# Kernel optimization log

Measured on AMD Instinct MI355X. Metric: run time of the kernel, lower is better.

The kernel has to match this reference:

```python
import jax, jax.numpy as jnp
import numpy as np

EPS = 1e-08


def setup_inputs() -> dict:
    key = jax.random.key(0)
    k1, = jax.random.split(key, 1)
    B, T, F = 64, 1000, 257
    mag = jax.random.uniform(k1, (B, T, F), dtype=jnp.float32)
    s = jnp.zeros((B, F), dtype=jnp.float32)
    weights = jnp.ones((1, 1, F), dtype=jnp.float32)
    bias = jnp.zeros((1, 1, F), dtype=jnp.float32)
    alpha = jnp.full((1, F), -4.0, dtype=jnp.float32)
    return {"mag": mag, "s": s, "weights": weights, "bias": bias, "alpha": alpha}


def reference(mag, s, weights, bias, alpha):
    # mag: [B, T, F]; s: [B, F] initial EMA state
    power = mag * mag                      # [B, T, F]
    a = jax.nn.sigmoid(alpha)              # [1, F], broadcasts over B

    def step(carry, p_t):
        # carry: [B, F], p_t: [B, F]
        new = carry * (1.0 - a) + p_t * a
        return new, new

    # scan over time axis: move T to leading axis
    _, smooth = jax.lax.scan(step, s, jnp.swapaxes(power, 0, 1))  # smooth: [T, B, F]
    smooth_data = jnp.sqrt(jnp.swapaxes(smooth, 0, 1))            # [B, T, F]
    return mag / (smooth_data + EPS) * weights + bias
```

## Files before the change

kernel.cpp:

```cpp
#include <hip/hip_runtime.h>

#define EPS 1e-8f

__device__ __forceinline__ float sigmoidf_(float x) {
    return 1.0f / (1.0f + expf(-x));
}


template <int L>
__global__ __launch_bounds__(256)
void fns12_aggregate(const float* __restrict__ mag,
                     const float* __restrict__ alpha,
                     float* __restrict__ S,
                     int B, int T, int F, int C1) {
    const int BF = B * F;
    int g = blockIdx.x * blockDim.x + threadIdx.x;
    if (g >= BF * C1) return;
    const int bf = g % BF;
    const int c  = g / BF;
    const int b  = bf / F;
    const int f  = bf - b * F;

    const float a   = sigmoidf_(alpha[f]);
    const float oma = 1.0f - a;

    const float* p = mag + ((size_t)b * T + (size_t)c * L) * F + f;

    float m[L];
#pragma unroll
    for (int t = 0; t < L; ++t)
        m[t] = p[(size_t)t * F];
    asm volatile("" ::: "memory");

    float local = 0.0f;
#pragma unroll
    for (int t = 0; t < L; ++t)
        local = local * oma + (m[t] * m[t]) * a;
    S[(size_t)c * BF + bf] = local;
}

template <int L, int C>
__global__ __launch_bounds__(256)
void fns12_emit(const float* __restrict__ mag,
                const float* __restrict__ s0,
                const float* __restrict__ weights,
                const float* __restrict__ bias,
                const float* __restrict__ alpha,
                const float* __restrict__ S,
                float* __restrict__ out,
                int B, int T, int F) {
    const int BF = B * F;
    int g = blockIdx.x * blockDim.x + threadIdx.x;
    if (g >= BF * C) return;
    const int bf = g % BF;
    const int c  = g / BF;
    const int b  = bf / F;
    const int f  = bf - b * F;

    const float a   = sigmoidf_(alpha[f]);
    const float oma = 1.0f - a;
    const float w   = weights[f];
    const float bi  = bias[f];

    const float* p = mag + ((size_t)b * T + (size_t)c * L) * F + f;
    float*       o = out + ((size_t)b * T + (size_t)c * L) * F + f;

    float m[L];
#pragma unroll
    for (int t = 0; t < L; ++t)
        m[t] = p[(size_t)t * F];

    float SS[C - 1];
#pragma unroll
    for (int j = 0; j < C - 1; ++j)
        SS[j] = (j < c) ? S[(size_t)j * BF + bf] : 0.0f;
    asm volatile("" ::: "memory");

    float D = 1.0f;
#pragma unroll
    for (int i = 0; i < L; ++i) D *= oma;
    float carry = s0[bf];
#pragma unroll
    for (int j = 0; j < C - 1; ++j)
        carry = (j < c) ? (carry * D + SS[j]) : carry;

#pragma unroll
    for (int t = 0; t < L; ++t) {
        carry = carry * oma + (m[t] * m[t]) * a;
        o[(size_t)t * F] = m[t] * __builtin_amdgcn_rcpf(sqrtf(carry) + EPS) * w + bi;
    }
}

template <int L>
__global__ __launch_bounds__(256)
void fns11_emit(const float* __restrict__ mag,
                const float* __restrict__ s0,
                const float* __restrict__ weights,
                const float* __restrict__ bias,
                const float* __restrict__ alpha,
                const float* __restrict__ S,
                float* __restrict__ out,
                int B, int T, int F, int C) {
    const int BF = B * F;
    int g = blockIdx.x * blockDim.x + threadIdx.x;
    if (g >= BF * C) return;
    const int bf = g % BF;
    const int c  = g / BF;
    const int b  = bf / F;
    const int f  = bf - b * F;

    const float a   = sigmoidf_(alpha[f]);
    const float oma = 1.0f - a;
    const float w   = weights[f];
    const float bi  = bias[f];

    float carry = s0[bf];
    if (c > 0) {
        float D = 1.0f;
#pragma unroll
        for (int i = 0; i < L; ++i) D *= oma;
        for (int j = 0; j < c; ++j)
            carry = carry * D + S[(size_t)j * BF + bf];
    }

    const float* p = mag + ((size_t)b * T + (size_t)c * L) * F + f;
    float*       o = out + ((size_t)b * T + (size_t)c * L) * F + f;

    float m[L];
#pragma unroll
    for (int t = 0; t < L; ++t)
        m[t] = p[(size_t)t * F];
    asm volatile("" ::: "memory");

#pragma unroll
    for (int t = 0; t < L; ++t) {
        carry = carry * oma + (m[t] * m[t]) * a;
        o[(size_t)t * F] = m[t] * __builtin_amdgcn_rcpf(sqrtf(carry) + EPS) * w + bi;
    }
}

__global__ void fns_fallback(const float* __restrict__ mag,
                             const float* __restrict__ s0,
                             const float* __restrict__ weights,
                             const float* __restrict__ bias,
                             const float* __restrict__ alpha,
                             float* __restrict__ out,
                             int B, int T, int F) {
    int bf = blockIdx.x * blockDim.x + threadIdx.x;
    int BF = B * F;
    if (bf >= BF) return;
    int b = bf / F;
    int f = bf - b * F;

    float a  = sigmoidf_(alpha[f]);
    float w  = weights[f];
    float bi = bias[f];

    float carry = s0[bf];
    const float* p = mag + (size_t)b * T * F + f;
    float*       o = out + (size_t)b * T * F + f;

    for (int t = 0; t < T; ++t) {
        float m = p[(size_t)t * F];
        carry = carry * (1.0f - a) + (m * m) * a;
        o[(size_t)t * F] = m / (sqrtf(carry) + EPS) * w + bi;
    }
}

extern "C" void kernel_launch(void* const* d_in, const int* in_sizes, int n_in,
                              void* d_out, int out_size, void* d_ws, size_t ws_size,
                              hipStream_t stream) {
    const float* mag     = (const float*)d_in[0];
    const float* s0      = (const float*)d_in[1];
    const float* weights = (const float*)d_in[2];
    const float* bias    = (const float*)d_in[3];
    const float* alpha   = (const float*)d_in[4];
    float* out = (float*)d_out;

    int F  = in_sizes[4];
    int BF = in_sizes[1];
    int B  = BF / F;
    int T  = in_sizes[0] / BF;

    constexpr int L = 50;
    if (T % L == 0) {
        int C  = T / L;
        int C1 = C - 1;
        size_t need = (size_t)C1 * BF * sizeof(float);
        if (C1 >= 1 && ws_size >= need) {
            float* S = (float*)d_ws;
            int n1 = BF * C1;
            int n2 = BF * C;
            fns12_aggregate<L><<<(n1 + 255) / 256, 256, 0, stream>>>(
                mag, alpha, S, B, T, F, C1);
            if (C == 20) {
                fns12_emit<L, 20><<<(n2 + 255) / 256, 256, 0, stream>>>(
                    mag, s0, weights, bias, alpha, S, out, B, T, F);
            } else {
                fns11_emit<L><<<(n2 + 255) / 256, 256, 0, stream>>>(
                    mag, s0, weights, bias, alpha, S, out, B, T, F, C);
            }
            return;
        }
    }

    int threads = 256;
    int blocks  = (BF + threads - 1) / threads;
    fns_fallback<<<blocks, threads, 0, stream>>>(mag, s0, weights, bias,
                                                 alpha, out, B, T, F);
}
```

Measured before the change: 42.57 us.

## Fuse chunked EMA scan aggregate and emit into one kernel with LDS carries

Replaces the two-kernel chunked scan (aggregate pass writing chunk sums to global, then emit pass re-reading mag) with a single kernel. Each block handles 16 (b,f) chains by 40 time chunks of 25 steps. Chunk aggregates go into shared memory, and after a barrier each thread composes its prefix carry and emits output from the values already in registers. This removes the second read of mag and the workspace round trip, and uses shorter chunks. In exchange the blocks are 640 threads with only 16 consecutive f per row, giving 64-byte coalesced segments, and a block-wide barrier sits between the load and emit phases.

```diff
diff --git a/kernel.cpp b/kernel.cpp
--- a/kernel.cpp
+++ b/kernel.cpp
@@ -4,6 +4,65 @@
 
 __device__ __forceinline__ float sigmoidf_(float x) {
     return 1.0f / (1.0f + expf(-x));
+}
+
+
+template <int CPB, int L, int C>
+__global__ __launch_bounds__(CPB * C)
+void fns14_fused(const float* __restrict__ mag,
+                 const float* __restrict__ s0,
+                 const float* __restrict__ weights,
+                 const float* __restrict__ bias,
+                 const float* __restrict__ alpha,
+                 float* __restrict__ out,
+                 int B, int T, int F) {
+    __shared__ float agg[C][CPB];
+
+    const int chainL = threadIdx.x % CPB;
+    const int chunk  = threadIdx.x / CPB;
+    const int bf = blockIdx.x * CPB + chainL;
+    const int b  = bf / F;
+    const int f  = bf - b * F;
+
+    const float a   = sigmoidf_(alpha[f]);
+    const float oma = 1.0f - a;
+
+    const float* p = mag + ((size_t)b * T + (size_t)chunk * L) * F + f;
+
+    float m[L];
+#pragma unroll
+    for (int t = 0; t < L; ++t)
+        m[t] = p[(size_t)t * F];
+    asm volatile("" ::: "memory");
+
+    float local = 0.0f;
+#pragma unroll
+    for (int t = 0; t < L; ++t)
+        local = local * oma + (m[t] * m[t]) * a;
+
+    agg[chunk][chainL] = local;
+    __syncthreads();
+
+    float D = 1.0f;
+#pragma unroll
+    for (int i = 0; i < L; ++i) D *= oma;
+
+    float carry = s0[bf];
+#pragma unroll
+    for (int j = 0; j < C - 1; ++j) {
+        float Sv = agg[j][chainL];
+        carry = (j < chunk) ? (carry * D + Sv) : carry;
+    }
+
+    const float w  = weights[f];
+    const float bi = bias[f];
+    float* o = out + ((size_t)b * T + (size_t)chunk * L) * F + f;
+
+#pragma unroll
+    for (int t = 0; t < L; ++t) {
+        carry = carry * oma + (m[t] * m[t]) * a;
+        o[(size_t)t * F] = m[t] * __builtin_amdgcn_rcpf(sqrtf(carry) + EPS) * w + bi;
+    }
 }
 
 
@@ -37,58 +96,6 @@
     for (int t = 0; t < L; ++t)
         local = local * oma + (m[t] * m[t]) * a;
     S[(size_t)c * BF + bf] = local;
-}
-
-template <int L, int C>
-__global__ __launch_bounds__(256)
-void fns12_emit(const float* __restrict__ mag,
-                const float* __restrict__ s0,
-                const float* __restrict__ weights,
-                const float* __restrict__ bias,
-                const float* __restrict__ alpha,
-                const float* __restrict__ S,
-                float* __restrict__ out,
-                int B, int T, int F) {
-    const int BF = B * F;
-    int g = blockIdx.x * blockDim.x + threadIdx.x;
-    if (g >= BF * C) return;
-    const int bf = g % BF;
-    const int c  = g / BF;
-    const int b  = bf / F;
-    const int f  = bf - b * F;
-
-    const float a   = sigmoidf_(alpha[f]);
-    const float oma = 1.0f - a;
-    const float w   = weights[f];
-    const float bi  = bias[f];
-
-    const float* p = mag + ((size_t)b * T + (size_t)c * L) * F + f;
-    float*       o = out + ((size_t)b * T + (size_t)c * L) * F + f;
-
-    float m[L];
-#pragma unroll
-    for (int t = 0; t < L; ++t)
-        m[t] = p[(size_t)t * F];
-
-    float SS[C - 1];
-#pragma unroll
-    for (int j = 0; j < C - 1; ++j)
-        SS[j] = (j < c) ? S[(size_t)j * BF + bf] : 0.0f;
-    asm volatile("" ::: "memory");
-
-    float D = 1.0f;
-#pragma unroll
-    for (int i = 0; i < L; ++i) D *= oma;
-    float carry = s0[bf];
-#pragma unroll
-    for (int j = 0; j < C - 1; ++j)
-        carry = (j < c) ? (carry * D + SS[j]) : carry;
-
-#pragma unroll
-    for (int t = 0; t < L; ++t) {
-        carry = carry * oma + (m[t] * m[t]) * a;
-        o[(size_t)t * F] = m[t] * __builtin_amdgcn_rcpf(sqrtf(carry) + EPS) * w + bi;
-    }
 }
 
 template <int L>
@@ -182,6 +189,16 @@
     int B  = BF / F;
     int T  = in_sizes[0] / BF;
 
+    constexpr int CPB = 16;
+    constexpr int LF  = 25;
+    constexpr int CF  = 40;
+    if (T == LF * CF && BF % CPB == 0) {
+        int blocks = BF / CPB;
+        fns14_fused<CPB, LF, CF><<<blocks, CPB * CF, 0, stream>>>(
+            mag, s0, weights, bias, alpha, out, B, T, F);
+        return;
+    }
+
     constexpr int L = 50;
     if (T % L == 0) {
         int C  = T / L;
@@ -193,13 +210,8 @@
             int n2 = BF * C;
             fns12_aggregate<L><<<(n1 + 255) / 256, 256, 0, stream>>>(
                 mag, alpha, S, B, T, F, C1);
-            if (C == 20) {
-                fns12_emit<L, 20><<<(n2 + 255) / 256, 256, 0, stream>>>(
-                    mag, s0, weights, bias, alpha, S, out, B, T, F);
-            } else {
-                fns11_emit<L><<<(n2 + 255) / 256, 256, 0, stream>>>(
-                    mag, s0, weights, bias, alpha, S, out, B, T, F, C);
-            }
+            fns11_emit<L><<<(n2 + 255) / 256, 256, 0, stream>>>(
+                mag, s0, weights, bias, alpha, S, out, B, T, F, C);
             return;
         }
     }
```

Measured after the change: 65.67 us. 1.54x slower.

## Split emit chunks into half-length sub-chunks using extra partial aggregates

Applied to the files above, without the earlier changes.

The aggregate kernel now reads all 20 chunks and also writes each chunk's partial EMA after its first 25 steps. The emit kernel runs twice as many threads, each covering 25 timesteps. Odd sub-chunks fold in the half-chunk partial to rebuild their starting state. This doubles emit parallelism and halves per-thread register arrays, which should raise occupancy, at the cost of the aggregate kernel reading the last chunk too and writing an extra workspace array.

```diff
diff --git a/kernel.cpp b/kernel.cpp
--- a/kernel.cpp
+++ b/kernel.cpp
@@ -4,6 +4,105 @@
 
 __device__ __forceinline__ float sigmoidf_(float x) {
     return 1.0f / (1.0f + expf(-x));
+}
+
+
+template <int L, int LH>
+__global__ __launch_bounds__(256)
+void fns16_aggregate(const float* __restrict__ mag,
+                     const float* __restrict__ alpha,
+                     float* __restrict__ S50,
+                     float* __restrict__ S25a,
+                     int B, int T, int F, int C) {
+    static_assert(L == 2 * LH, "");
+    const int BF = B * F;
+    int g = blockIdx.x * blockDim.x + threadIdx.x;
+    if (g >= BF * C) return;
+    const int bf = g % BF;
+    const int c  = g / BF;
+    const int b  = bf / F;
+    const int f  = bf - b * F;
+
+    const float a   = sigmoidf_(alpha[f]);
+    const float oma = 1.0f - a;
+
+    const float* p = mag + ((size_t)b * T + (size_t)c * L) * F + f;
+
+    float m[L];
+#pragma unroll
+    for (int t = 0; t < L; ++t)
+        m[t] = p[(size_t)t * F];
+    asm volatile("" ::: "memory");
+
+    float local = 0.0f;
+#pragma unroll
+    for (int t = 0; t < LH; ++t)
+        local = local * oma + (m[t] * m[t]) * a;
+    S25a[(size_t)c * BF + bf] = local;
+#pragma unroll
+    for (int t = LH; t < L; ++t)
+        local = local * oma + (m[t] * m[t]) * a;
+    if (c < C - 1)
+        S50[(size_t)c * BF + bf] = local;
+}
+
+template <int LH, int C>
+__global__ __launch_bounds__(256)
+void fns16_emit(const float* __restrict__ mag,
+                const float* __restrict__ s0,
+                const float* __restrict__ weights,
+                const float* __restrict__ bias,
+                const float* __restrict__ alpha,
+                const float* __restrict__ S50,
+                const float* __restrict__ S25a,
+                float* __restrict__ out,
+                int B, int T, int F) {
+    const int BF = B * F;
+    int g = blockIdx.x * blockDim.x + threadIdx.x;
+    if (g >= BF * 2 * C) return;
+    const int bf = g % BF;
+    const int sc = g / BF;
+    const int c   = sc >> 1;
+    const int odd = sc & 1;
+    const int b  = bf / F;
+    const int f  = bf - b * F;
+
+    const float a   = sigmoidf_(alpha[f]);
+    const float oma = 1.0f - a;
+    const float w   = weights[f];
+    const float bi  = bias[f];
+
+    const float* p = mag + ((size_t)b * T + (size_t)sc * LH) * F + f;
+    float*       o = out + ((size_t)b * T + (size_t)sc * LH) * F + f;
+
+    float SS[C - 1];
+#pragma unroll
+    for (int j = 0; j < C - 1; ++j)
+        SS[j] = (j < c) ? S50[(size_t)j * BF + bf] : 0.0f;
+    float extra = odd ? S25a[(size_t)c * BF + bf] : 0.0f;
+
+    float m[LH];
+#pragma unroll
+    for (int t = 0; t < LH; ++t)
+        m[t] = p[(size_t)t * F];
+    asm volatile("" ::: "memory");
+
+    float D25 = 1.0f;
+#pragma unroll
+    for (int i = 0; i < LH; ++i) D25 *= oma;
+    const float D50 = D25 * D25;
+
+    float carry = s0[bf];
+#pragma unroll
+    for (int j = 0; j < C - 1; ++j)
+        carry = (j < c) ? (carry * D50 + SS[j]) : carry;
+    carry = odd ? (carry * D25 + extra) : carry;
+
+#pragma unroll
+    for (int t = 0; t < LH; ++t) {
+        carry = carry * oma + (m[t] * m[t]) * a;
+        o[(size_t)t * F] = m[t] * __builtin_amdgcn_rcpf(sqrtf(carry) + EPS) * w + bi;
+    }
 }
 
 
@@ -37,58 +136,6 @@
     for (int t = 0; t < L; ++t)
         local = local * oma + (m[t] * m[t]) * a;
     S[(size_t)c * BF + bf] = local;
-}
-
-template <int L, int C>
-__global__ __launch_bounds__(256)
-void fns12_emit(const float* __restrict__ mag,
-                const float* __restrict__ s0,
-                const float* __restrict__ weights,
-                const float* __restrict__ bias,
-                const float* __restrict__ alpha,
-                const float* __restrict__ S,
-                float* __restrict__ out,
-                int B, int T, int F) {
-    const int BF = B * F;
-    int g = blockIdx.x * blockDim.x + threadIdx.x;
-    if (g >= BF * C) return;
-    const int bf = g % BF;
-    const int c  = g / BF;
-    const int b  = bf / F;
-    const int f  = bf - b * F;
-
-    const float a   = sigmoidf_(alpha[f]);
-    const float oma = 1.0f - a;
-    const float w   = weights[f];
-    const float bi  = bias[f];
-
-    const float* p = mag + ((size_t)b * T + (size_t)c * L) * F + f;
-    float*       o = out + ((size_t)b * T + (size_t)c * L) * F + f;
-
-    float m[L];
-#pragma unroll
-    for (int t = 0; t < L; ++t)
-        m[t] = p[(size_t)t * F];
-
-    float SS[C - 1];
-#pragma unroll
-    for (int j = 0; j < C - 1; ++j)
-        SS[j] = (j < c) ? S[(size_t)j * BF + bf] : 0.0f;
-    asm volatile("" ::: "memory");
-
-    float D = 1.0f;
-#pragma unroll
-    for (int i = 0; i < L; ++i) D *= oma;
-    float carry = s0[bf];
-#pragma unroll
-    for (int j = 0; j < C - 1; ++j)
-        carry = (j < c) ? (carry * D + SS[j]) : carry;
-
-#pragma unroll
-    for (int t = 0; t < L; ++t) {
-        carry = carry * oma + (m[t] * m[t]) * a;
-        o[(size_t)t * F] = m[t] * __builtin_amdgcn_rcpf(sqrtf(carry) + EPS) * w + bi;
-    }
 }
 
 template <int L>
@@ -182,9 +229,26 @@
     int B  = BF / F;
     int T  = in_sizes[0] / BF;
 
-    constexpr int L = 50;
+    constexpr int L  = 50;
+    constexpr int LH = 25;
     if (T % L == 0) {
-        int C  = T / L;
+        int C = T / L;
+        if (C == 20) {
+            size_t s50Bytes = (size_t)(C - 1) * BF * sizeof(float);
+            size_t aOff     = (s50Bytes + 255) & ~(size_t)255;
+            size_t need     = aOff + (size_t)C * BF * sizeof(float);
+            if (ws_size >= need) {
+                float* S50  = (float*)d_ws;
+                float* S25a = (float*)((char*)d_ws + aOff);
+                int n1 = BF * C;
+                int n2 = BF * 2 * C;
+                fns16_aggregate<L, LH><<<(n1 + 255) / 256, 256, 0, stream>>>(
+                    mag, alpha, S50, S25a, B, T, F, C);
+                fns16_emit<LH, 20><<<(n2 + 255) / 256, 256, 0, stream>>>(
+                    mag, s0, weights, bias, alpha, S50, S25a, out, B, T, F);
+                return;
+            }
+        }
         int C1 = C - 1;
         size_t need = (size_t)C1 * BF * sizeof(float);
         if (C1 >= 1 && ws_size >= need) {
@@ -193,13 +257,8 @@
             int n2 = BF * C;
             fns12_aggregate<L><<<(n1 + 255) / 256, 256, 0, stream>>>(
                 mag, alpha, S, B, T, F, C1);
-            if (C == 20) {
-                fns12_emit<L, 20><<<(n2 + 255) / 256, 256, 0, stream>>>(
-                    mag, s0, weights, bias, alpha, S, out, B, T, F);
-            } else {
-                fns11_emit<L><<<(n2 + 255) / 256, 256, 0, stream>>>(
-                    mag, s0, weights, bias, alpha, S, out, B, T, F, C);
-            }
+            fns11_emit<L><<<(n2 + 255) / 256, 256, 0, stream>>>(
+                mag, s0, weights, bias, alpha, S, out, B, T, F, C);
             return;
         }
     }
```

Measured after the change: 44.28 us. +4.0%, slower.
